# Performance work log

Measured on AMD Instinct MI355X. Metric: run time of the kernel, lower is better.

## Reference

```python
import jax, jax.numpy as jnp
import numpy as np

EMBED = 896
HQ = 16      # query heads
HK = 4       # kv heads
D = EMBED // HQ          # 56 head dim
KV_EMBED = D * HK        # 224
G = HQ // HK             # 4 groups per kv head
LN_EPS = 1e-5


def setup_inputs() -> dict:
    key = jax.random.key(0)
    ks = jax.random.split(key, 8)
    b, n = 2, 2048
    inp = {
        "query": jax.random.normal(ks[0], (b, n, EMBED), jnp.float32),
        "key":   jax.random.normal(ks[1], (b, n, EMBED), jnp.float32),
        "value": jax.random.normal(ks[2], (b, n, EMBED), jnp.float32),
        # torch Linear weights are (out_features, in_features), y = x @ W.T
        "Wq": jax.random.normal(ks[3], (EMBED, EMBED), jnp.float32) * 0.02,
        "Wk": jax.random.normal(ks[4], (KV_EMBED, EMBED), jnp.float32) * 0.02,
        "Wv": jax.random.normal(ks[5], (KV_EMBED, EMBED), jnp.float32) * 0.02,
        "Wo": jax.random.normal(ks[6], (EMBED, EMBED), jnp.float32) * 0.02,
        "ln_gamma": jnp.ones((EMBED,), jnp.float32),
        "ln_beta": jnp.zeros((EMBED,), jnp.float32),
    }
    return inp


def _layer_norm(x, gamma, beta):
    mu = jnp.mean(x, axis=-1, keepdims=True)
    var = jnp.var(x, axis=-1, keepdims=True)
    return (x - mu) * jax.lax.rsqrt(var + LN_EPS) * gamma + beta


def reference(query, key, value, Wq, Wk, Wv, Wo, ln_gamma, ln_beta):
    b, n, _ = query.shape
    s = key.shape[1]
    # projections
    q = query @ Wq.T                      # (b, n, EMBED)
    k = key @ Wk.T                        # (b, s, KV_EMBED)
    v = value @ Wv.T                      # (b, s, KV_EMBED)
    # split heads: q -> (b, hk, g, n, d); k, v -> (b, hk, s, d)
    q = q.reshape(b, n, HQ, D).transpose(0, 2, 1, 3)      # (b, hq, n, d)
    q = q.reshape(b, HK, G, n, D)                          # (b, hk, g, n, d)
    k = k.reshape(b, s, HK, D).transpose(0, 2, 1, 3)       # (b, hk, s, d)
    v = v.reshape(b, s, HK, D).transpose(0, 2, 1, 3)       # (b, hk, s, d)
    # scaled scores
    scale = jnp.asarray(D, q.dtype) ** 0.5
    scores = jnp.einsum('bhgnd,bhsd->bhgns', q, k) / scale  # (b, hk, g, n, s)
    # causal mask
    mask = jnp.tril(jnp.ones((n, s), bool))                # (n, s)
    scores = jnp.where(mask, scores, jnp.asarray(-jnp.inf, scores.dtype))
    attn = jax.nn.softmax(scores, axis=-1)                 # (b, hk, g, n, s)
    # (dropout is identity in deterministic eval-mode reference)
    out = jnp.einsum('bhgns,bhsd->bhgnd', attn, v)         # (b, hk, g, n, d)
    # merge heads back: (h g) ordering matches the query split
    out = out.transpose(0, 3, 1, 2, 4).reshape(b, n, EMBED)  # b n (h g d)
    out = _layer_norm(out, ln_gamma, ln_beta)
    out = out @ Wo.T                                        # (b, n, EMBED)
    # need_weights + average_attn_weights: b h g n s -> b n s (h g), mean over n
    aw = attn.transpose(0, 3, 4, 1, 2).reshape(b, n, s, HQ).mean(axis=1)  # (b, s, hq)
    return out, aw
```

## Files before the change

kernel.cpp:

```cpp
#include <hip/hip_runtime.h>

#define B_    2
#define N_    2048
#define EMBED 896
#define HQ    16
#define HK    4
#define D_    56
#define DP    64

typedef unsigned short u16;
typedef unsigned int   u32;
typedef __attribute__((ext_vector_type(8))) short bf16x8;
typedef __attribute__((ext_vector_type(4))) float f32x4;

__device__ __forceinline__ u16 f2bf(float f) {
  u32 u = __builtin_bit_cast(u32, f);
  return (u16)((u + 0x7FFFu + ((u >> 16) & 1u)) >> 16);
}

__device__ __forceinline__ u32 cvtpk_bf16(float lo, float hi) {
  u32 r;
  asm("v_cvt_pk_bf16_f32 %0, %1, %2" : "=v"(r) : "v"(lo), "v"(hi));
  return r;
}

#define EXP2F(x) __builtin_amdgcn_exp2f(x)

__device__ __forceinline__ void gload_lds16(const u16* g, u16* l) {
  __builtin_amdgcn_global_load_lds(
      (const __attribute__((address_space(1))) void*)g,
      (__attribute__((address_space(3))) void*)l, 16, 0, 0);
}

#define QSCALE 0.19278822f

#define SEG_IN  3670016u
#define SEG_WQ  802816u
#define SEG_WK  200704u

__global__ __launch_bounds__(256) void to_bf16(
    const float* __restrict__ q, const float* __restrict__ k,
    const float* __restrict__ v, const float* __restrict__ wq,
    const float* __restrict__ wk, const float* __restrict__ wv,
    const float* __restrict__ wo, u16* __restrict__ qb, u16* __restrict__ kb,
    u16* __restrict__ vb, u16* __restrict__ wqb, u16* __restrict__ wkb,
    u16* __restrict__ wvb, u16* __restrict__ wob) {
  size_t e = ((size_t)blockIdx.x * 256 + threadIdx.x) * 4;
  const float* src;
  u16* dst;
  size_t off;
  if (e < SEG_IN)            { src = q;  dst = qb;  off = e; }
  else if (e < 2 * (size_t)SEG_IN) { src = k;  dst = kb;  off = e - SEG_IN; }
  else if (e < 3 * (size_t)SEG_IN) { src = v;  dst = vb;  off = e - 2 * (size_t)SEG_IN; }
  else {
    size_t r = e - 3 * (size_t)SEG_IN;
    if (r < SEG_WQ)                    { src = wq; dst = wqb; off = r; }
    else if (r < SEG_WQ + SEG_WK)      { src = wk; dst = wkb; off = r - SEG_WQ; }
    else if (r < SEG_WQ + 2 * SEG_WK)  { src = wv; dst = wvb; off = r - SEG_WQ - SEG_WK; }
    else                               { src = wo; dst = wob; off = r - SEG_WQ - 2 * SEG_WK; }
  }
  float4 v4 = *(const float4*)(src + off);
  uint2 pb;
  pb.x = (u32)f2bf(v4.x) | ((u32)f2bf(v4.y) << 16);
  pb.y = (u32)f2bf(v4.z) | ((u32)f2bf(v4.w) << 16);
  *(uint2*)(dst + off) = pb;
}

#define NT_K 14

#define GEMM_CORE(APTR, WPTR)                                                  \
  for (int it = 0; it < NT_K; ++it) {                                          \
    const int k0 = it * 64;                                                    \
    {                                                                          \
      const u16* Ag = (APTR) + (size_t)m0 * EMBED + k0;                        \
      _Pragma("unroll") for (int i = 0; i < 4; i++) {                          \
        int f = i * 256 + t;                                                   \
        int r = f >> 3, s = (f & 7) ^ (r & 7);                                 \
        gload_lds16(Ag + (size_t)r * EMBED + s * 8,                            \
                    AsL + (i * 256 + fwbase) * 8);                             \
      }                                                                        \
      const u16* Wg = (WPTR) + (size_t)wn0 * EMBED + k0;                       \
      _Pragma("unroll") for (int i = 0; i < 2; i++) {                          \
        int f = i * 256 + t;                                                   \
        int r = f >> 3, s = (f & 7) ^ (r & 7);                                 \
        gload_lds16(Wg + (size_t)r * EMBED + s * 8,                            \
                    BsL + (i * 256 + fwbase) * 8);                             \
      }                                                                        \
    }                                                                          \
    __syncthreads();                  \
    _Pragma("unroll") for (int kk = 0; kk < 2; kk++) {                         \
      bf16x8 af[2], bfv[4];                                                    \
      _Pragma("unroll") for (int mf = 0; mf < 2; mf++) {                       \
        int ra = wr + mf * 16 + fr;                                            \
        af[mf] =                                                               \
            *(const bf16x8*)&AsL[ra * 64 + ((fg + kk * 4) ^ (ra & 7)) * 8];    \
      }                                                                        \
      _Pragma("unroll") for (int nf = 0; nf < 4; nf++) {                       \
        int rb = nf * 16 + fr;                                                 \
        bfv[nf] =                                                              \
            *(const bf16x8*)&BsL[rb * 64 + ((fg + kk * 4) ^ (rb & 7)) * 8];    \
      }                                                                        \
      _Pragma("unroll") for (int mf = 0; mf < 2; mf++)                         \
          _Pragma("unroll") for (int nf = 0; nf < 4; nf++)                     \
              acc[mf][nf] = __builtin_amdgcn_mfma_f32_16x16x32_bf16(           \
                  af[mf], bfv[nf], acc[mf][nf], 0, 0, 0);                      \
    }                                                                          \
    __syncthreads();         \
  }

__global__ __launch_bounds__(256) void proj_gemm(
    const u16* __restrict__ qb, const u16* __restrict__ kb,
    const u16* __restrict__ vb, const u16* __restrict__ Wqb,
    const u16* __restrict__ Wkb, const u16* __restrict__ Wvb,
    u16* __restrict__ Qp, u16* __restrict__ Kp, u16* __restrict__ Vt) {
  __shared__ __align__(16) u16 lds[12288];
  u16* AsL = lds;
  u16* BsL = lds + 8192;
  const int t = threadIdx.x;
  const int m0 = blockIdx.x * 128;
  const int y = blockIdx.y;
  int p, nt;
  if (y < 14)      { p = 0; nt = y; }
  else if (y < 18) { p = 1; nt = y - 14; }
  else             { p = 2; nt = y - 18; }
  const u16* A = p == 0 ? qb : (p == 1 ? kb : vb);
  const u16* W = p == 0 ? Wqb : (p == 1 ? Wkb : Wvb);
  const int Nproj = p == 0 ? 896 : 224;
  const int wn0 = nt * 64;

  const int w = t >> 6, lane = t & 63;
  const int fr = lane & 15, fg = lane >> 4;
  const int wr = w * 32;
  const int fwbase = t & 192;

  f32x4 acc[2][4] = {};

  GEMM_CORE(A, W)

  if (p < 2) {
#pragma unroll
    for (int nf = 0; nf < 4; nf++) {
      int col = wn0 + nf * 16 + fr;
      if (col < Nproj) {
        int hh = col / 56, d = col - hh * 56;
#pragma unroll
        for (int mf = 0; mf < 2; mf++)
#pragma unroll
          for (int r = 0; r < 4; r++) {
            int row = m0 + wr + mf * 16 + fg * 4 + r;
            int bb = row >> 11, nn = row & 2047;
            float vv = acc[mf][nf][r];
            if (p == 0)
              Qp[((size_t)((bb * 16 + hh) * 2048 + nn)) * 64 + d] =
                  f2bf(vv * QSCALE);
            else
              Kp[((size_t)((bb * 4 + hh) * 2048 + nn)) * 64 + d] = f2bf(vv);
          }
      }
    }
  } else {
    u16* Traw = lds;
#define TS(r_, c_) Traw[(r_)*136 + (c_)]
#pragma unroll
    for (int nf = 0; nf < 4; nf++)
#pragma unroll
      for (int mf = 0; mf < 2; mf++)
#pragma unroll
        for (int r = 0; r < 4; r++)
          TS(nf * 16 + fr, wr + mf * 16 + fg * 4 + r) = f2bf(acc[mf][nf][r]);
    __syncthreads();
    const int bb = m0 >> 11, n_base = m0 & 2047;
#pragma unroll
    for (int i = 0; i < 4; i++) {
      int flat = i * 256 + t;
      int dr = flat >> 4;
      int c8 = (flat & 15) * 8;
      int col = wn0 + dr;
      if (col < 224) {
        int hh = col / 56, d = col - hh * 56;
        *(int4*)(Vt + ((size_t)((bb * 4 + hh) * 64 + d)) * 2048 + n_base + c8) =
            *(int4*)&TS(dr, c8);
      }
    }
  }
}

__global__ __launch_bounds__(256) void gemm_wo(const u16* __restrict__ A,
                                               const u16* __restrict__ W,
                                               float* __restrict__ C) {
  __shared__ __align__(16) u16 lds[12288];
  u16* AsL = lds;
  u16* BsL = lds + 8192;
  const int t = threadIdx.x;
  const int m0 = blockIdx.x * 128;
  const int wn0 = blockIdx.y * 64;
  const int w = t >> 6, lane = t & 63;
  const int fr = lane & 15, fg = lane >> 4;
  const int wr = w * 32;
  const int fwbase = t & 192;

  f32x4 acc[2][4] = {};

  GEMM_CORE(A, W)

#pragma unroll
  for (int nf = 0; nf < 4; nf++) {
    int col = wn0 + nf * 16 + fr;
#pragma unroll
    for (int mf = 0; mf < 2; mf++)
#pragma unroll
      for (int r = 0; r < 4; r++) {
        int row = m0 + wr + mf * 16 + fg * 4 + r;
        C[(size_t)row * EMBED + col] = acc[mf][nf][r];
      }
  }
}

__global__ __launch_bounds__(256) void attn_fwd(const u16* __restrict__ Qp,
                                                const u16* __restrict__ Kp,
                                                const u16* __restrict__ Vt,
                                                float* __restrict__ AO,
                                                float* __restrict__ linv_g) {
  const int p = blockIdx.x, hk = blockIdx.y, b = blockIdx.z;
  const int t = threadIdx.x, w = t >> 6, lane = t & 63;
  const int fr = lane & 15, fg = lane >> 4;
  const int h = hk * 4 + w;

  __shared__ __align__(16) u16 KVs[2][2][4096];
  __shared__ __align__(16) u16 Ps[4][16][72];

  const u16* Qh = Qp + (size_t)(b * HQ + h) * N_ * DP;
  const u16* Kh = Kp + (size_t)(b * HK + hk) * N_ * DP;
  const u16* Vh = Vt + (size_t)(b * HK + hk) * DP * N_;
  float* linv_h = linv_g + (size_t)(b * HQ + h) * N_;

  const int fwb = t & 192;
  const int fx = fr & 7;

#define ISSUE_KV(ntt_, buf_)                                                   \
  {                                                                            \
    const u16* Kb = Kh + (size_t)(ntt_)*64 * DP;                               \
    const u16* Vb = Vh + (ntt_)*64;                                            \
    _Pragma("unroll") for (int i = 0; i < 2; i++) {                            \
      int f = i * 256 + t;                                                     \
      int r = f >> 3, sl = (f & 7) ^ (r & 7);                                  \
      gload_lds16(Kb + (size_t)r * DP + sl * 8,                                \
                  &KVs[buf_][0][(i * 256 + fwb) * 8]);                         \
      gload_lds16(Vb + (size_t)r * N_ + sl * 8,                                \
                  &KVs[buf_][1][(i * 256 + fwb) * 8]);                         \
    }                                                                          \
  }

  int bi = 0;
  ISSUE_KV(0, 0);

  for (int half = 0; half < 2; ++half) {
    const int s = half ? (127 - p) : p;
    const int nt = (s >> 2) + 1;

    bf16x8 qf[2];
#pragma unroll
    for (int kk = 0; kk < 2; kk++)
      qf[kk] = *(const bf16x8*)(Qh + (size_t)(s * 16 + fr) * DP +
                                kk * 32 + fg * 8);

    f32x4 oacc[4] = {};
    float l_acc[4] = {};

    for (int tt = 0; tt < nt; ++tt) {
      __syncthreads();
      {
        int ntt = tt + 1;
        bool more = true;
        if (ntt == nt) {
          if (half == 1) more = false;
          else ntt = 0;
        }
        if (more) ISSUE_KV(ntt, bi ^ 1);
      }

      f32x4 sacc[4] = {};
#pragma unroll
      for (int kk = 0; kk < 2; kk++) {
        bf16x8 bk[4];
#pragma unroll
        for (int jf = 0; jf < 4; jf++)
          bk[jf] = *(const bf16x8*)&KVs[bi][0][(jf * 16 + fr) * 64 +
                                               ((kk * 4 + fg) ^ fx) * 8];
#pragma unroll
        for (int jf = 0; jf < 4; jf++)
          sacc[jf] = __builtin_amdgcn_mfma_f32_16x16x32_bf16(
              qf[kk], bk[jf], sacc[jf], 0, 0, 0);
      }

      if (tt == nt - 1) {
#pragma unroll
        for (int jf = 0; jf < 4; jf++) {
          int gj = tt * 64 + jf * 16 + fr;
          float pv[4];
#pragma unroll
          for (int r = 0; r < 4; r++) {
            int gi = s * 16 + fg * 4 + r;
            pv[r] = (gj <= gi) ? EXP2F(sacc[jf][r]) : 0.f;
            l_acc[r] += pv[r];
          }
          u32 w01 = cvtpk_bf16(pv[0], pv[1]);
          u32 w23 = cvtpk_bf16(pv[2], pv[3]);
          Ps[w][fg * 4 + 0][jf * 16 + fr] = (u16)w01;
          Ps[w][fg * 4 + 1][jf * 16 + fr] = (u16)(w01 >> 16);
          Ps[w][fg * 4 + 2][jf * 16 + fr] = (u16)w23;
          Ps[w][fg * 4 + 3][jf * 16 + fr] = (u16)(w23 >> 16);
        }
      } else {
#pragma unroll
        for (int jf = 0; jf < 4; jf++) {
          float pv[4];
#pragma unroll
          for (int r = 0; r < 4; r++) {
            pv[r] = EXP2F(sacc[jf][r]);
            l_acc[r] += pv[r];
          }
          u32 w01 = cvtpk_bf16(pv[0], pv[1]);
          u32 w23 = cvtpk_bf16(pv[2], pv[3]);
          Ps[w][fg * 4 + 0][jf * 16 + fr] = (u16)w01;
          Ps[w][fg * 4 + 1][jf * 16 + fr] = (u16)(w01 >> 16);
          Ps[w][fg * 4 + 2][jf * 16 + fr] = (u16)w23;
          Ps[w][fg * 4 + 3][jf * 16 + fr] = (u16)(w23 >> 16);
        }
      }

#pragma unroll
      for (int kk = 0; kk < 2; kk++) {
        bf16x8 ap = *(const bf16x8*)&Ps[w][fr][kk * 32 + fg * 8];
        bf16x8 bv[4];
#pragma unroll
        for (int df = 0; df < 4; df++)
          bv[df] = *(const bf16x8*)&KVs[bi][1][(df * 16 + fr) * 64 +
                                               ((kk * 4 + fg) ^ fx) * 8];
#pragma unroll
        for (int df = 0; df < 4; df++)
          oacc[df] = __builtin_amdgcn_mfma_f32_16x16x32_bf16(
              ap, bv[df], oacc[df], 0, 0, 0);
      }
      bi ^= 1;
    }

#pragma unroll
    for (int r = 0; r < 4; r++) {
      float v = l_acc[r];
      v += __shfl_xor(v, 1);
      v += __shfl_xor(v, 2);
      v += __shfl_xor(v, 4);
      v += __shfl_xor(v, 8);
      l_acc[r] = 1.0f / v;
    }
#pragma unroll
    for (int df = 0; df < 4; df++) {
      int d = df * 16 + fr;
      if (d < D_) {
#pragma unroll
        for (int r = 0; r < 4; r++) {
          int gi = s * 16 + fg * 4 + r;
          AO[((size_t)b * N_ + gi) * EMBED + h * D_ + d] =
              oacc[df][r] * l_acc[r];
        }
      }
    }
    if (fr == 0) {
#pragma unroll
      for (int r = 0; r < 4; r++)
        linv_h[s * 16 + fg * 4 + r] = l_acc[r];
    }
  }
}

struct QTile {
  bf16x8 q[4][2];
  float li[4];
};

#define LOADQ(dst, rt_)                                                        \
  {                                                                            \
    _Pragma("unroll") for (int ifr = 0; ifr < 4; ifr++) {                      \
      _Pragma("unroll") for (int kk = 0; kk < 2; kk++)                         \
          dst.q[ifr][kk] = *(const bf16x8*)(Qh +                               \
              (size_t)((rt_)*64 + ifr * 16 + fr) * DP + kk * 32 + fg * 8);     \
      dst.li[ifr] = linv_h[(rt_)*64 + ifr * 16 + fr];                          \
    }                                                                          \
  }

#define COMPUTET(src, rt_)                                                     \
  {                                                                            \
    f32x4 tacc[2][4] = {};                                                     \
    _Pragma("unroll") for (int kk = 0; kk < 2; kk++)                           \
        _Pragma("unroll") for (int jm = 0; jm < 2; jm++)                       \
        _Pragma("unroll") for (int ifr = 0; ifr < 4; ifr++)                    \
            tacc[jm][ifr] = __builtin_amdgcn_mfma_f32_16x16x32_bf16(           \
                kf[jm][kk], src.q[ifr][kk], tacc[jm][ifr], 0, 0, 0);           \
    if ((rt_) == rt0) {                                                        \
      _Pragma("unroll") for (int jm = 0; jm < 2; jm++)                         \
          _Pragma("unroll") for (int ifr = 0; ifr < 4; ifr++)                  \
          _Pragma("unroll") for (int r = 0; r < 4; r++) {                      \
        int gi = (rt_)*64 + ifr * 16 + fr;                                     \
        int gj = ct * 32 + jm * 16 + fg * 4 + r;                               \
        if (gi >= gj)                                                          \
          s_acc[jm][r] += EXP2F(tacc[jm][ifr][r]) * src.li[ifr];               \
      }                                                                        \
    } else {                                                                   \
      _Pragma("unroll") for (int jm = 0; jm < 2; jm++)                         \
          _Pragma("unroll") for (int ifr = 0; ifr < 4; ifr++)                  \
          _Pragma("unroll") for (int r = 0; r < 4; r++)                        \
              s_acc[jm][r] += EXP2F(tacc[jm][ifr][r]) * src.li[ifr];           \
    }                                                                          \
  }

__global__ __launch_bounds__(256) void attn_aw(const u16* __restrict__ Qp,
                                               const u16* __restrict__ Kp,
                                               const float* __restrict__ linv_g,
                                               float* __restrict__ aw) {
  const int p = blockIdx.x, h = blockIdx.y, b = blockIdx.z;
  const int hk = h >> 2;
  const int t = threadIdx.x, w = t >> 6, lane = t & 63;
  const int fr = lane & 15, fg = lane >> 4;

  __shared__ float red[2][4][32];

  const u16* Qh = Qp + (size_t)(b * HQ + h) * N_ * DP;
  const u16* Kh = Kp + (size_t)(b * HK + hk) * N_ * DP;
  const float* linv_h = linv_g + (size_t)(b * HQ + h) * N_;

  for (int half = 0; half < 2; ++half) {
    const int ct = half ? (63 - p) : p;
    const int rt0 = ct >> 1;

    bf16x8 kf[2][2];
#pragma unroll
    for (int jm = 0; jm < 2; jm++)
#pragma unroll
      for (int kk = 0; kk < 2; kk++)
        kf[jm][kk] = *(const bf16x8*)(Kh + (size_t)(ct * 32 + jm * 16 + fr) * DP +
                                      kk * 32 + fg * 8);

    float s_acc[2][4] = {};
    QTile qa, qb;
    int rt = rt0 + w;
    if (rt <= 31) {
      LOADQ(qa, rt);
      while (true) {
        if (rt + 4 <= 31) LOADQ(qb, rt + 4);
        COMPUTET(qa, rt);
        rt += 4;
        if (rt > 31) break;
        if (rt + 4 <= 31) LOADQ(qa, rt + 4);
        COMPUTET(qb, rt);
        rt += 4;
        if (rt > 31) break;
      }
    }

#pragma unroll
    for (int jm = 0; jm < 2; jm++)
#pragma unroll
      for (int r = 0; r < 4; r++) {
        float v = s_acc[jm][r];
        v += __shfl_xor(v, 1);
        v += __shfl_xor(v, 2);
        v += __shfl_xor(v, 4);
        v += __shfl_xor(v, 8);
        if (fr == 0) red[half][w][jm * 16 + fg * 4 + r] = v;
      }
  }

  __syncthreads();
  if (w == 0 && fr == 0) {
#pragma unroll
    for (int half = 0; half < 2; ++half) {
      const int ct = half ? (63 - p) : p;
#pragma unroll
      for (int jm = 0; jm < 2; jm++)
#pragma unroll
        for (int r = 0; r < 4; r++) {
          int idx = jm * 16 + fg * 4 + r;
          float v = red[half][0][idx] + red[half][1][idx] +
                    red[half][2][idx] + red[half][3][idx];
          int gj = ct * 32 + jm * 16 + fg * 4 + r;
          aw[((size_t)b * N_ + gj) * HQ + h] = v * (1.0f / N_);
        }
    }
  }
}

__global__ __launch_bounds__(256) void ln_fwd(const float* __restrict__ AO,
                                              const float* __restrict__ gamma,
                                              const float* __restrict__ beta,
                                              u16* __restrict__ out) {
  const int row = blockIdx.x;
  const float* x = AO + (size_t)row * EMBED;
  const int t = threadIdx.x;
  float s = 0.f, s2 = 0.f;
  float v[4];
#pragma unroll
  for (int i = 0; i < 4; i++) {
    int c = t + 256 * i;
    v[i] = (c < EMBED) ? x[c] : 0.f;
    s += v[i];
    s2 += v[i] * v[i];
  }
#pragma unroll
  for (int m = 1; m <= 32; m <<= 1) {
    s += __shfl_xor(s, m);
    s2 += __shfl_xor(s2, m);
  }
  __shared__ float red[8];
  const int w = t >> 6, lane = t & 63;
  if (lane == 0) {
    red[w] = s;
    red[4 + w] = s2;
  }
  __syncthreads();
  s = red[0] + red[1] + red[2] + red[3];
  s2 = red[4] + red[5] + red[6] + red[7];
  const float mu = s * (1.0f / EMBED);
  const float var = s2 * (1.0f / EMBED) - mu * mu;
  const float rs = rsqrtf(var + 1e-5f);
#pragma unroll
  for (int i = 0; i < 4; i++) {
    int c = t + 256 * i;
    if (c < EMBED)
      out[(size_t)row * EMBED + c] = f2bf((v[i] - mu) * rs * gamma[c] + beta[c]);
  }
}

extern "C" void kernel_launch(void* const* d_in, const int* in_sizes, int n_in,
                              void* d_out, int out_size, void* d_ws,
                              size_t ws_size, hipStream_t stream) {
  (void)in_sizes; (void)n_in; (void)out_size; (void)ws_size;
  const float* query = (const float*)d_in[0];
  const float* key   = (const float*)d_in[1];
  const float* value = (const float*)d_in[2];
  const float* Wq    = (const float*)d_in[3];
  const float* Wk    = (const float*)d_in[4];
  const float* Wv    = (const float*)d_in[5];
  const float* Wo    = (const float*)d_in[6];
  const float* gamma = (const float*)d_in[7];
  const float* beta  = (const float*)d_in[8];

  float* out = (float*)d_out;
  float* aw  = out + (size_t)B_ * N_ * EMBED;

  char* ws = (char*)d_ws;
  u16* Qp = (u16*)ws;        ws += (size_t)B_ * HQ * N_ * DP * 2;
  u16* Kp = (u16*)ws;        ws += (size_t)B_ * HK * N_ * DP * 2;
  u16* Vt = (u16*)ws;        ws += (size_t)B_ * HK * N_ * DP * 2;
  float* linv = (float*)ws;  ws += (size_t)B_ * HQ * N_ * 4;
  u16* Wqb = (u16*)ws;       ws += (size_t)SEG_WQ * 2;
  u16* Wkb = (u16*)ws;       ws += (size_t)SEG_WK * 2;
  u16* Wvb = (u16*)ws;       ws += (size_t)SEG_WK * 2;
  u16* Wob = (u16*)ws;       ws += (size_t)SEG_WQ * 2;
  char* region = ws;
  u16* qb = (u16*)region;
  u16* kb = qb + (size_t)SEG_IN;
  u16* vb = kb + (size_t)SEG_IN;
  float* AO = (float*)region;
  u16* LNo = (u16*)(region + (size_t)B_ * N_ * EMBED * 4);

  const size_t pad_bytes =
      ((size_t)B_ * HQ * N_ * DP + 2 * (size_t)B_ * HK * N_ * DP) * 2;
  (void)hipMemsetAsync(Qp, 0, pad_bytes, stream);

  dim3 blk(256);
  const int M = B_ * N_;

  to_bf16<<<dim3(12712), blk, 0, stream>>>(query, key, value, Wq, Wk, Wv, Wo,
                                           qb, kb, vb, Wqb, Wkb, Wvb, Wob);

  proj_gemm<<<dim3(M / 128, 22), blk, 0, stream>>>(qb, kb, vb, Wqb, Wkb, Wvb,
                                                   Qp, Kp, Vt);

  attn_fwd<<<dim3(64, HK, B_), blk, 0, stream>>>(Qp, Kp, Vt, AO, linv);
  attn_aw<<<dim3(32, HQ, B_), blk, 0, stream>>>(Qp, Kp, linv, aw);

  ln_fwd<<<dim3(M), blk, 0, stream>>>(AO, gamma, beta, LNo);
  gemm_wo<<<dim3(M / 128, 14), blk, 0, stream>>>(LNo, Wob, out);
}
```

Measured before the change: 141.3 us.

## Split attention KV range across two blocks and merge partials in layernorm

The attention forward grid is doubled: each block handles half of the key tiles for its query rows and writes unnormalized bf16 partial outputs plus partial row sums. The layernorm kernel now merges the two partials, computes the reciprocal normaliser, and writes linv for the attention-weights kernel, which is reordered to run after it. This targets low occupancy, since the old grid had only 512 blocks, in exchange for extra partial-output traffic and bf16 rounding of the partials. The P scratch buffer in LDS also gets an XOR swizzle in place of padding to avoid bank conflicts.

```diff
diff --git a/kernel.cpp b/kernel.cpp
--- a/kernel.cpp
+++ b/kernel.cpp
@@ -16,6 +16,11 @@
 __device__ __forceinline__ u16 f2bf(float f) {
   u32 u = __builtin_bit_cast(u32, f);
   return (u16)((u + 0x7FFFu + ((u >> 16) & 1u)) >> 16);
+}
+
+__device__ __forceinline__ float bf2f(u16 x) {
+  u32 u = (u32)x << 16;
+  return __builtin_bit_cast(float, u);
 }
 
 __device__ __forceinline__ u32 cvtpk_bf16(float lo, float hi) {
@@ -219,26 +224,28 @@
 __global__ __launch_bounds__(256) void attn_fwd(const u16* __restrict__ Qp,
                                                 const u16* __restrict__ Kp,
                                                 const u16* __restrict__ Vt,
-                                                float* __restrict__ AO,
-                                                float* __restrict__ linv_g) {
-  const int p = blockIdx.x, hk = blockIdx.y, b = blockIdx.z;
+                                                u16* __restrict__ Op,
+                                                float* __restrict__ lp) {
+  const int p = blockIdx.x, hk = blockIdx.y;
+  const int b = blockIdx.z >> 1, sg = blockIdx.z & 1;
   const int t = threadIdx.x, w = t >> 6, lane = t & 63;
   const int fr = lane & 15, fg = lane >> 4;
   const int h = hk * 4 + w;
 
   __shared__ __align__(16) u16 KVs[2][2][4096];
-  __shared__ __align__(16) u16 Ps[4][16][72];
+  __shared__ __align__(16) u16 Ps[4 * 16 * 64];
 
   const u16* Qh = Qp + (size_t)(b * HQ + h) * N_ * DP;
   const u16* Kh = Kp + (size_t)(b * HK + hk) * N_ * DP;
   const u16* Vh = Vt + (size_t)(b * HK + hk) * DP * N_;
-  float* linv_h = linv_g + (size_t)(b * HQ + h) * N_;
 
   const int fwb = t & 192;
   const int fx = fr & 7;
 
+#define PSW(w_, row_, col8_) ((w_)*1024 + (row_)*64 + (((col8_) ^ ((row_)&7)) * 8))
+
 #define ISSUE_KV(ntt_, buf_)                                                   \
-  {                                                                            \
+  do {                                                                         \
     const u16* Kb = Kh + (size_t)(ntt_)*64 * DP;                               \
     const u16* Vb = Vh + (ntt_)*64;                                            \
     _Pragma("unroll") for (int i = 0; i < 2; i++) {                            \
@@ -249,14 +256,24 @@
       gload_lds16(Vb + (size_t)r * N_ + sl * 8,                                \
                   &KVs[buf_][1][(i * 256 + fwb) * 8]);                         \
     }                                                                          \
-  }
+  } while (0)
+
+  const int s0 = p, s1 = 127 - p;
+  const int ntf0 = (s0 >> 2) + 1, ntf1 = (s1 >> 2) + 1;
+  const int lo0 = sg ? (ntf0 >> 1) : 0, hi0 = sg ? ntf0 : (ntf0 >> 1);
+  const int lo1 = sg ? (ntf1 >> 1) : 0, hi1 = sg ? ntf1 : (ntf1 >> 1);
 
   int bi = 0;
-  ISSUE_KV(0, 0);
+  if (hi0 > lo0) {
+    ISSUE_KV(lo0, 0);
+  } else if (hi1 > lo1) {
+    ISSUE_KV(lo1, 0);
+  }
 
   for (int half = 0; half < 2; ++half) {
-    const int s = half ? (127 - p) : p;
-    const int nt = (s >> 2) + 1;
+    const int s = half ? s1 : s0;
+    const int ntf = half ? ntf1 : ntf0;
+    const int lo = half ? lo1 : lo0, hi = half ? hi1 : hi0;
 
     bf16x8 qf[2];
 #pragma unroll
@@ -267,16 +284,15 @@
     f32x4 oacc[4] = {};
     float l_acc[4] = {};
 
-    for (int tt = 0; tt < nt; ++tt) {
+    for (int tt = lo; tt < hi; ++tt) {
       __syncthreads();
       {
-        int ntt = tt + 1;
-        bool more = true;
-        if (ntt == nt) {
-          if (half == 1) more = false;
-          else ntt = 0;
+        int ntt = -1;
+        if (tt + 1 < hi) ntt = tt + 1;
+        else if (half == 0 && hi1 > lo1) ntt = lo1;
+        if (ntt >= 0) {
+          ISSUE_KV(ntt, bi ^ 1);
         }
-        if (more) ISSUE_KV(ntt, bi ^ 1);
       }
 
       f32x4 sacc[4] = {};
@@ -293,7 +309,7 @@
               qf[kk], bk[jf], sacc[jf], 0, 0, 0);
       }
 
-      if (tt == nt - 1) {
+      if (tt == ntf - 1) {
 #pragma unroll
         for (int jf = 0; jf < 4; jf++) {
           int gj = tt * 64 + jf * 16 + fr;
@@ -306,10 +322,11 @@
           }
           u32 w01 = cvtpk_bf16(pv[0], pv[1]);
           u32 w23 = cvtpk_bf16(pv[2], pv[3]);
-          Ps[w][fg * 4 + 0][jf * 16 + fr] = (u16)w01;
-          Ps[w][fg * 4 + 1][jf * 16 + fr] = (u16)(w01 >> 16);
-          Ps[w][fg * 4 + 2][jf * 16 + fr] = (u16)w23;
-          Ps[w][fg * 4 + 3][jf * 16 + fr] = (u16)(w23 >> 16);
+          int c8 = jf * 2 + (fr >> 3), c7 = fr & 7;
+          Ps[PSW(w, fg * 4 + 0, c8) + c7] = (u16)w01;
+          Ps[PSW(w, fg * 4 + 1, c8) + c7] = (u16)(w01 >> 16);
+          Ps[PSW(w, fg * 4 + 2, c8) + c7] = (u16)w23;
+          Ps[PSW(w, fg * 4 + 3, c8) + c7] = (u16)(w23 >> 16);
         }
       } else {
 #pragma unroll
@@ -322,16 +339,17 @@
           }
           u32 w01 = cvtpk_bf16(pv[0], pv[1]);
           u32 w23 = cvtpk_bf16(pv[2], pv[3]);
-          Ps[w][fg * 4 + 0][jf * 16 + fr] = (u16)w01;
-          Ps[w][fg * 4 + 1][jf * 16 + fr] = (u16)(w01 >> 16);
-          Ps[w][fg * 4 + 2][jf * 16 + fr] = (u16)w23;
-          Ps[w][fg * 4 + 3][jf * 16 + fr] = (u16)(w23 >> 16);
+          int c8 = jf * 2 + (fr >> 3), c7 = fr & 7;
+          Ps[PSW(w, fg * 4 + 0, c8) + c7] = (u16)w01;
+          Ps[PSW(w, fg * 4 + 1, c8) + c7] = (u16)(w01 >> 16);
+          Ps[PSW(w, fg * 4 + 2, c8) + c7] = (u16)w23;
+          Ps[PSW(w, fg * 4 + 3, c8) + c7] = (u16)(w23 >> 16);
         }
       }
 
 #pragma unroll
       for (int kk = 0; kk < 2; kk++) {
-        bf16x8 ap = *(const bf16x8*)&Ps[w][fr][kk * 32 + fg * 8];
+        bf16x8 ap = *(const bf16x8*)&Ps[PSW(w, fr, kk * 4 + fg)];
         bf16x8 bv[4];
 #pragma unroll
         for (int df = 0; df < 4; df++)
@@ -352,24 +370,22 @@
       v += __shfl_xor(v, 2);
       v += __shfl_xor(v, 4);
       v += __shfl_xor(v, 8);
-      l_acc[r] = 1.0f / v;
-    }
+      l_acc[r] = v;
+    }
+    const size_t obase = (((size_t)(sg * 2 + b) * 16 + h) * 2048 + s * 16);
 #pragma unroll
     for (int df = 0; df < 4; df++) {
       int d = df * 16 + fr;
       if (d < D_) {
 #pragma unroll
-        for (int r = 0; r < 4; r++) {
-          int gi = s * 16 + fg * 4 + r;
-          AO[((size_t)b * N_ + gi) * EMBED + h * D_ + d] =
-              oacc[df][r] * l_acc[r];
-        }
+        for (int r = 0; r < 4; r++)
+          Op[(obase + fg * 4 + r) * 56 + d] = f2bf(oacc[df][r]);
       }
     }
     if (fr == 0) {
 #pragma unroll
       for (int r = 0; r < 4; r++)
-        linv_h[s * 16 + fg * 4 + r] = l_acc[r];
+        lp[obase + fg * 4 + r] = l_acc[r];
     }
   }
 }
@@ -490,19 +506,40 @@
   }
 }
 
-__global__ __launch_bounds__(256) void ln_fwd(const float* __restrict__ AO,
+__global__ __launch_bounds__(256) void ln_fwd(const u16* __restrict__ Op,
+                                              const float* __restrict__ lp,
                                               const float* __restrict__ gamma,
                                               const float* __restrict__ beta,
-                                              u16* __restrict__ out) {
+                                              u16* __restrict__ out,
+                                              float* __restrict__ linv_g) {
   const int row = blockIdx.x;
-  const float* x = AO + (size_t)row * EMBED;
+  const int b = row >> 11, n = row & 2047;
   const int t = threadIdx.x;
+  __shared__ float lrec[16];
+  __shared__ float red[8];
+
+  if (t < 16) {
+    float l0 = lp[((size_t)(0 + b) * 16 + t) * 2048 + n];
+    float l1 = lp[((size_t)(2 + b) * 16 + t) * 2048 + n];
+    float ri = 1.0f / (l0 + l1);
+    lrec[t] = ri;
+    linv_g[((size_t)b * 16 + t) * 2048 + n] = ri;
+  }
+  __syncthreads();
+
   float s = 0.f, s2 = 0.f;
   float v[4];
 #pragma unroll
   for (int i = 0; i < 4; i++) {
     int c = t + 256 * i;
-    v[i] = (c < EMBED) ? x[c] : 0.f;
+    if (c < EMBED) {
+      int h = c / 56, d = c - h * 56;
+      size_t o0 = (((size_t)(0 + b) * 16 + h) * 2048 + n) * 56 + d;
+      size_t o1 = (((size_t)(2 + b) * 16 + h) * 2048 + n) * 56 + d;
+      v[i] = (bf2f(Op[o0]) + bf2f(Op[o1])) * lrec[h];
+    } else {
+      v[i] = 0.f;
+    }
     s += v[i];
     s2 += v[i] * v[i];
   }
@@ -511,7 +548,6 @@
     s += __shfl_xor(s, m);
     s2 += __shfl_xor(s2, m);
   }
-  __shared__ float red[8];
   const int w = t >> 6, lane = t & 63;
   if (lane == 0) {
     red[w] = s;
@@ -553,6 +589,7 @@
   u16* Kp = (u16*)ws;        ws += (size_t)B_ * HK * N_ * DP * 2;
   u16* Vt = (u16*)ws;        ws += (size_t)B_ * HK * N_ * DP * 2;
   float* linv = (float*)ws;  ws += (size_t)B_ * HQ * N_ * 4;
+  float* lp   = (float*)ws;  ws += (size_t)4 * HQ * N_ * 4;
   u16* Wqb = (u16*)ws;       ws += (size_t)SEG_WQ * 2;
   u16* Wkb = (u16*)ws;       ws += (size_t)SEG_WK * 2;
   u16* Wvb = (u16*)ws;       ws += (size_t)SEG_WK * 2;
@@ -561,8 +598,8 @@
   u16* qb = (u16*)region;
   u16* kb = qb + (size_t)SEG_IN;
   u16* vb = kb + (size_t)SEG_IN;
-  float* AO = (float*)region;
-  u16* LNo = (u16*)(region + (size_t)B_ * N_ * EMBED * 4);
+  u16* Op  = (u16*)region;
+  u16* LNo = Op + (size_t)4 * HQ * N_ * 56;
 
   const size_t pad_bytes =
       ((size_t)B_ * HQ * N_ * DP + 2 * (size_t)B_ * HK * N_ * DP) * 2;
@@ -577,9 +614,9 @@
   proj_gemm<<<dim3(M / 128, 22), blk, 0, stream>>>(qb, kb, vb, Wqb, Wkb, Wvb,
                                                    Qp, Kp, Vt);
 
-  attn_fwd<<<dim3(64, HK, B_), blk, 0, stream>>>(Qp, Kp, Vt, AO, linv);
+  attn_fwd<<<dim3(64, HK, B_ * 2), blk, 0, stream>>>(Qp, Kp, Vt, Op, lp);
+  ln_fwd<<<dim3(M), blk, 0, stream>>>(Op, lp, gamma, beta, LNo, linv);
+
   attn_aw<<<dim3(32, HQ, B_), blk, 0, stream>>>(Qp, Kp, linv, aw);
-
-  ln_fwd<<<dim3(M), blk, 0, stream>>>(AO, gamma, beta, LNo);
   gemm_wo<<<dim3(M / 128, 14), blk, 0, stream>>>(LNo, Wob, out);
 }
```

After: 140.4 us. No clear change (-0.6%).
